# Optimization experiments

Hardware: AMD Instinct MI355X
Metric: run time of the kernel (lower is better)

Reference implementation:

```python
import jax, jax.numpy as jnp
import numpy as np
import math

B, S, HID = 2, 2048, 1024
NH, HD = 16, 64
MAX_SEQ = 65536  # RoPE base from RotaryEmbedding


def _rope_tables(seq_len, dim):
    inv_freq = 1.0 / (MAX_SEQ ** (jnp.arange(0, dim, 2, dtype=jnp.float32) / dim))
    t = jnp.arange(seq_len, dtype=jnp.float32)
    freqs = jnp.einsum('i,j->ij', t, inv_freq)          # [S, dim/2]
    emb = jnp.concatenate([freqs, freqs], axis=-1)      # [S, dim]
    return jnp.cos(emb), jnp.sin(emb)


def _rotate_half(x):
    x1, x2 = jnp.split(x, 2, axis=-1)
    return jnp.concatenate([-x2, x1], axis=-1)


def setup_inputs() -> dict:
    key = jax.random.key(0)
    ks = jax.random.split(key, 9)
    std_qkv = 1.0 / math.sqrt(NH * HD)
    std_o = 1.0 / math.sqrt(HID)
    return {
        'input_embeds': jax.random.normal(ks[0], (B, S, HID), dtype=jnp.float32),
        'Wq': jax.random.normal(ks[1], (NH * HD, HID), dtype=jnp.float32) * std_qkv,
        'bq': jnp.zeros((NH * HD,), dtype=jnp.float32),
        'Wk': jax.random.normal(ks[2], (NH * HD, HID), dtype=jnp.float32) * std_qkv,
        'bk': jnp.zeros((NH * HD,), dtype=jnp.float32),
        'Wv': jax.random.normal(ks[3], (NH * HD, HID), dtype=jnp.float32) * std_qkv,
        'bv': jnp.zeros((NH * HD,), dtype=jnp.float32),
        'Wo': jax.random.normal(ks[4], (HID, NH * HD), dtype=jnp.float32) * std_o,
        'bo': jnp.zeros((HID,), dtype=jnp.float32),
    }


def reference(input_embeds, Wq, bq, Wk, bk, Wv, bv, Wo, bo):
    x = input_embeds
    b, s, _ = x.shape
    # QKV projections (torch Linear: x @ W.T + b)
    q = x @ Wq.T + bq
    k = x @ Wk.T + bk
    v = x @ Wv.T + bv
    # [B, S, NH*HD] -> [B, NH, S, HD]
    q = q.reshape(b, s, NH, HD).transpose(0, 2, 1, 3)
    k = k.reshape(b, s, NH, HD).transpose(0, 2, 1, 3)
    v = v.reshape(b, s, NH, HD).transpose(0, 2, 1, 3)
    # RoPE
    cos, sin = _rope_tables(s, HD)  # [S, HD]
    q = q * cos + _rotate_half(q) * sin
    k = k * cos + _rotate_half(k) * sin
    # SDPA (non-causal, no mask)
    scale = 1.0 / math.sqrt(HD)
    scores = jnp.einsum('bhqd,bhkd->bhqk', q, k) * scale
    attn = jax.nn.softmax(scores, axis=-1)
    out = jnp.einsum('bhqk,bhkd->bhqd', attn, v)
    # [B, NH, S, HD] -> [B, S, NH*HD]
    out = out.transpose(0, 2, 1, 3).reshape(b, s, NH * HD)
    return out @ Wo.T + bo
```

## Files before the change

### kernel.cpp

```cpp
#include <hip/hip_runtime.h>
#include <cstdint>
#include <cstddef>

#define S_LEN 2048
#define NHEAD 16
#define HDIM  64
#define HID_  1024

typedef short s8v  __attribute__((ext_vector_type(8)));
typedef short s4v  __attribute__((ext_vector_type(4)));
typedef float f4v  __attribute__((ext_vector_type(4)));
typedef float f16v __attribute__((ext_vector_type(16)));

__device__ __forceinline__ short f2b(float x) {
    union { float f; unsigned u; } a; a.f = x;
    unsigned r = a.u + 0x7fffu + ((a.u >> 16) & 1u);
    return (short)(r >> 16);
}
__device__ __forceinline__ float b2f(short x) {
    union { unsigned u; float f; } a; a.u = ((unsigned)(unsigned short)x) << 16;
    return a.f;
}

__device__ __forceinline__ void gload_lds16(const void* g, void* l) {
    __builtin_amdgcn_global_load_lds(
        (__attribute__((address_space(1))) void*)const_cast<void*>(g),
        (__attribute__((address_space(3))) void*)l, 16, 0, 0);
}

__device__ __forceinline__ unsigned cvtpk(float a, float b) {
    unsigned r;
    asm("v_cvt_pk_bf16_f32 %0, %1, %2" : "=v"(r) : "v"(a), "v"(b));
    return r;
}
__device__ __forceinline__ void plswap(unsigned& a, unsigned& b) {
    asm("v_permlane32_swap_b32 %0, %1" : "+v"(a), "+v"(b));
}

__global__ __launch_bounds__(256) void prep_kernel(
    const float* __restrict__ X,
    const float* __restrict__ Wq, const float* __restrict__ Wk,
    const float* __restrict__ Wv, const float* __restrict__ Wo,
    short* __restrict__ Xb, short* __restrict__ Wcat, short* __restrict__ Wob,
    float2* __restrict__ rtab)
{
    const int bid = blockIdx.x;
    if (bid < 8192) {
        const float* src;
        short* dst;
        int i;
        if (bid < 4096) {
            src = X; dst = Xb; i = bid * 256 + threadIdx.x;
        } else {
            int w = (bid - 4096) >> 10;
            src = (w == 0) ? Wq : (w == 1) ? Wk : (w == 2) ? Wv : Wo;
            dst = (w < 3) ? (Wcat + (size_t)w * 1048576) : Wob;
            i = ((bid - 4096) & 1023) * 256 + threadIdx.x;
        }
        float4 v = reinterpret_cast<const float4*>(src)[i];
        s4v o;
        o[0] = f2b(v.x); o[1] = f2b(v.y); o[2] = f2b(v.z); o[3] = f2b(v.w);
        reinterpret_cast<s4v*>(dst)[i] = o;
    } else {
        int idx = (bid - 8192) * 256 + threadIdx.x;
        int s = idx >> 5, j = idx & 31;
        float inv = exp2f(-0.5f * (float)j);
        float ang = (float)s * inv;
        float2 cs; cs.x = cosf(ang); cs.y = sinf(ang);
        rtab[idx] = cs;
    }
}

__global__ __launch_bounds__(256) void gemm_qkv(
    const short* __restrict__ A, const short* __restrict__ Bw,
    const float* __restrict__ bq, const float* __restrict__ bk,
    const float* __restrict__ bv,
    short* __restrict__ Qo, short* __restrict__ Ko, short* __restrict__ Vo,
    const float2* __restrict__ rtab)
{
    __shared__ short Asl[2][128 * 32];
    __shared__ short Bsl[2][128 * 32];
    const int t = threadIdx.x;
    const int lane = t & 63;
    const int l15 = lane & 15, l4 = lane >> 4;
    const int wid = t >> 6;
    const int blk = blockIdx.x;
    const int x = blk & 7, j = blk >> 3;
    const int tn = (x * 3 + j % 3) * 128;
    const int tm = (j / 3) * 128;
    const int K = 1024;
    const int wrow = (wid >> 1) * 64, wcol = (wid & 1) * 64;

    f4v acc[4][4];
#pragma unroll
    for (int i = 0; i < 4; ++i)
#pragma unroll
        for (int jj = 0; jj < 4; ++jj) acc[i][jj] = (f4v){0.f, 0.f, 0.f, 0.f};

    const int r0 = t >> 2;
    const int c0 = (t & 3) * 8;
    const int wbase = (t & ~63) * 8;

#define QSTAGE(buf, kt) do { const int k0_ = (kt) << 5;                            \
        gload_lds16(A  + (size_t)(tm + r0)      * K + k0_ + c0, &Asl[buf][wbase]);        \
        gload_lds16(A  + (size_t)(tm + 64 + r0) * K + k0_ + c0, &Asl[buf][2048 + wbase]); \
        gload_lds16(Bw + (size_t)(tn + r0)      * K + k0_ + c0, &Bsl[buf][wbase]);        \
        gload_lds16(Bw + (size_t)(tn + 64 + r0) * K + k0_ + c0, &Bsl[buf][2048 + wbase]); \
    } while (0)

    QSTAGE(0, 0);
    int cur = 0;
    for (int kt = 0; kt < 32; ++kt) {
        if (kt < 31) {
            QSTAGE(cur ^ 1, kt + 1);
            asm volatile("s_waitcnt vmcnt(4)" ::: "memory");
        } else {
            asm volatile("s_waitcnt vmcnt(0)" ::: "memory");
        }
        __builtin_amdgcn_s_barrier();
        __builtin_amdgcn_sched_barrier(0);
        s8v af[4], bf[4];
#pragma unroll
        for (int i = 0; i < 4; ++i) {
            af[i] = *(const s8v*)&Asl[cur][(wrow + i * 16 + l15) * 32 + 8 * l4];
            bf[i] = *(const s8v*)&Bsl[cur][(wcol + i * 16 + l15) * 32 + 8 * l4];
        }
#pragma unroll
        for (int i = 0; i < 4; ++i)
#pragma unroll
            for (int jj = 0; jj < 4; ++jj)
                acc[i][jj] = __builtin_amdgcn_mfma_f32_16x16x32_bf16(af[i], bf[jj], acc[i][jj], 0, 0, 0);
        __builtin_amdgcn_s_barrier();
        cur ^= 1;
    }
#undef QSTAGE

    const int mode = tn >> 10;
    const float* bias = (mode == 0) ? bq : (mode == 1) ? bk : bv;
    short* outb = (mode == 0) ? Qo : (mode == 1) ? Ko : Vo;

    if (mode == 2) {
#pragma unroll
        for (int i = 0; i < 4; ++i) {
            int rowb = tm + wrow + i * 16 + l4 * 4;
            int b_ = rowb >> 11, s0 = rowb & 2047;
#pragma unroll
            for (int jj = 0; jj < 4; ++jj) {
                int col = tn + wcol + jj * 16 + l15;
                int cm = col & 1023;
                float bvv = bias[cm];
                int h = cm >> 6, d = col & 63;
                s4v o4;
#pragma unroll
                for (int r = 0; r < 4; ++r) o4[r] = f2b(acc[i][jj][r] + bvv);
                *(s4v*)&outb[((size_t)((b_ * NHEAD + h) * 64 + d)) * S_LEN + s0] = o4;
            }
        }
    } else {
        int h = ((tn & 1023) + wcol) >> 6;
        const float osc = (mode == 0) ? 0.180336880111f : 1.0f;
#pragma unroll
        for (int i = 0; i < 4; ++i) {
#pragma unroll
            for (int r = 0; r < 4; ++r) {
                int row = tm + wrow + i * 16 + l4 * 4 + r;
                int b_ = row >> 11, s = row & 2047;
                float2 cs0 = rtab[(s << 5) + l15];
                float2 cs1 = rtab[(s << 5) + 16 + l15];
#pragma unroll
                for (int jj = 0; jj < 4; ++jj) {
                    int col = tn + wcol + jj * 16 + l15;
                    int cm = col & 1023;
                    int d = col & 63;
                    float v  = acc[i][jj][r]     + bias[cm];
                    float vp = acc[i][jj ^ 2][r] + bias[cm ^ 32];
                    float2 cs = (jj & 1) ? cs1 : cs0;
                    float res = (d < 32) ? (v * cs.x - vp * cs.y)
                                         : (v * cs.x + vp * cs.y);
                    outb[(((size_t)(b_ * NHEAD + h) * S_LEN + s) << 6) + d] = f2b(res * osc);
                }
            }
        }
    }
}

__global__ __launch_bounds__(256) void gemm_o(
    const short* __restrict__ A, const short* __restrict__ Bw,
    const float* __restrict__ bias, float* __restrict__ outf)
{
    __shared__ short Asl[2][64 * 32];
    __shared__ short Bsl[2][128 * 32];
    const int t = threadIdx.x;
    const int lane = t & 63;
    const int l15 = lane & 15, l4 = lane >> 4;
    const int wid = t >> 6;
    const int blk = blockIdx.x;
    const int tn = (blk & 7) * 128;
    const int tm = (blk >> 3) * 64;
    const int K = 1024, N = 1024;
    const int wrow = (wid >> 1) * 32, wcol = (wid & 1) * 64;

    f4v acc[2][4];
#pragma unroll
    for (int i = 0; i < 2; ++i)
#pragma unroll
        for (int jj = 0; jj < 4; ++jj) acc[i][jj] = (f4v){0.f, 0.f, 0.f, 0.f};

    const int r0 = t >> 2;
    const int c0 = (t & 3) * 8;
    const int wbase = (t & ~63) * 8;

#define OSTAGE(buf, kt) do { const int k0_ = (kt) << 5;                            \
        gload_lds16(A  + (size_t)(tm + r0)      * K + k0_ + c0, &Asl[buf][wbase]);        \
        gload_lds16(Bw + (size_t)(tn + r0)      * K + k0_ + c0, &Bsl[buf][wbase]);        \
        gload_lds16(Bw + (size_t)(tn + 64 + r0) * K + k0_ + c0, &Bsl[buf][2048 + wbase]); \
    } while (0)

    OSTAGE(0, 0);
    int cur = 0;
    for (int kt = 0; kt < 32; ++kt) {
        if (kt < 31) {
            OSTAGE(cur ^ 1, kt + 1);
            asm volatile("s_waitcnt vmcnt(3)" ::: "memory");
        } else {
            asm volatile("s_waitcnt vmcnt(0)" ::: "memory");
        }
        __builtin_amdgcn_s_barrier();
        __builtin_amdgcn_sched_barrier(0);
        s8v af[2], bf[4];
#pragma unroll
        for (int i = 0; i < 2; ++i)
            af[i] = *(const s8v*)&Asl[cur][(wrow + i * 16 + l15) * 32 + 8 * l4];
#pragma unroll
        for (int jj = 0; jj < 4; ++jj)
            bf[jj] = *(const s8v*)&Bsl[cur][(wcol + jj * 16 + l15) * 32 + 8 * l4];
#pragma unroll
        for (int i = 0; i < 2; ++i)
#pragma unroll
            for (int jj = 0; jj < 4; ++jj)
                acc[i][jj] = __builtin_amdgcn_mfma_f32_16x16x32_bf16(af[i], bf[jj], acc[i][jj], 0, 0, 0);
        __builtin_amdgcn_s_barrier();
        cur ^= 1;
    }
#undef OSTAGE

#pragma unroll
    for (int i = 0; i < 2; ++i) {
        int rowb = tm + wrow + i * 16 + l4 * 4;
#pragma unroll
        for (int jj = 0; jj < 4; ++jj) {
            int col = tn + wcol + jj * 16 + l15;
            float bv = bias[col];
#pragma unroll
            for (int r = 0; r < 4; ++r)
                outf[(size_t)(rowb + r) * N + col] = acc[i][jj][r] + bv;
        }
    }
}

#define SWB(row, bofs) ((bofs) ^ (((row) & 7) << 4))

__global__ __launch_bounds__(256, 4) void attn_split(
    const short* __restrict__ Q, const short* __restrict__ K,
    const short* __restrict__ Vt,
    short* __restrict__ P0, short* __restrict__ P1, float2* __restrict__ ML)
{
    __shared__ short Kl[4096];
    __shared__ short Vl[4096];

    const int t = threadIdx.x, lane = t & 63;
    const int wid = t >> 6;
    const int q5 = lane & 31, hi = lane >> 5;

    const int blk = blockIdx.x;
    const int x = blk & 7, j = blk >> 3;
    const int bh = x * 4 + (j & 3);
    const int rest = j >> 2;
    const int qb = rest & 15, split = rest >> 4;
    const int kt0 = split * 16;

    const short* Qb = Q + (size_t)bh * S_LEN * 64;
    const char*  Kb = (const char*)(K  + (size_t)bh * S_LEN * 64);
    const char*  Vb = (const char*)(Vt + (size_t)bh * S_LEN * 64);
    const int qrow = qb * 128 + wid * 32 + q5;

    s8v qf[4];
#pragma unroll
    for (int sl = 0; sl < 4; ++sl)
        qf[sl] = *(const s8v*)&Qb[(size_t)qrow * 64 + sl * 16 + hi * 8];

    f16v oacc[2];
#pragma unroll
    for (int dt = 0; dt < 2; ++dt)
#pragma unroll
        for (int e = 0; e < 16; ++e) oacc[dt][e] = 0.f;
    float m2 = -1e30f, lsum = 0.f;

    const int skey  = t >> 3;
    const int sboff = (t & 7) * 16;
    const int sw    = SWB(skey, sboff);
    const size_t kgoff = (size_t)skey * 128  + sboff;
    const size_t vgoff = (size_t)skey * 4096 + sboff;
    char* KlB = (char*)Kl;
    char* VlB = (char*)Vl;
    const int w0 = skey * 128 + sw;
    const int w1 = w0 + 32 * 128;

    {
        const size_t kbB = (size_t)kt0 * 64 * 128;
        const size_t vbB = (size_t)kt0 * 64 * 2;
        s8v g0 = *(const s8v*)(Kb + kbB + kgoff);
        s8v g1 = *(const s8v*)(Kb + kbB + kgoff + 32 * 128);
        s8v g2 = *(const s8v*)(Vb + vbB + vgoff);
        s8v g3 = *(const s8v*)(Vb + vbB + vgoff + 32 * 4096);
        *(s8v*)(KlB + w0) = g0; *(s8v*)(KlB + w1) = g1;
        *(s8v*)(VlB + w0) = g2; *(s8v*)(VlB + w1) = g3;
    }
    __syncthreads();

    for (int kt = kt0; kt < kt0 + 16; ++kt) {
        s8v g0, g1, g2, g3;
        const bool pre = (kt < kt0 + 15);
        if (pre) {
            const size_t kbB = (size_t)(kt + 1) * 64 * 128;
            const size_t vbB = (size_t)(kt + 1) * 64 * 2;
            g0 = *(const s8v*)(Kb + kbB + kgoff);
            g1 = *(const s8v*)(Kb + kbB + kgoff + 32 * 128);
            g2 = *(const s8v*)(Vb + vbB + vgoff);
            g3 = *(const s8v*)(Vb + vbB + vgoff + 32 * 4096);
        }

        f16v sc[2];
#pragma unroll
        for (int e = 0; e < 16; ++e) { sc[0][e] = 0.f; sc[1][e] = 0.f; }
        {
            const int kr0 = q5, kr1 = 32 + q5;
            const char* kb0 = KlB + kr0 * 128;
            const char* kb1 = KlB + kr1 * 128;
            __builtin_amdgcn_s_setprio(1);
#pragma unroll
            for (int sl = 0; sl < 4; ++sl) {
                s8v kf0 = *(const s8v*)(kb0 + SWB(kr0, sl * 32 + hi * 16));
                s8v kf1 = *(const s8v*)(kb1 + SWB(kr1, sl * 32 + hi * 16));
                sc[0] = __builtin_amdgcn_mfma_f32_32x32x16_bf16(kf0, qf[sl], sc[0], 0, 0, 0);
                sc[1] = __builtin_amdgcn_mfma_f32_32x32x16_bf16(kf1, qf[sl], sc[1], 0, 0, 0);
            }
            __builtin_amdgcn_s_setprio(0);
        }

        float m8[8];
#pragma unroll
        for (int e = 0; e < 8; ++e)
            m8[e] = fmaxf(fmaxf(sc[0][e], sc[0][e + 8]), fmaxf(sc[1][e], sc[1][e + 8]));
        float pm = fmaxf(fmaxf(fmaxf(m8[0], m8[4]), fmaxf(m8[1], m8[5])),
                         fmaxf(fmaxf(m8[2], m8[6]), fmaxf(m8[3], m8[7])));
        pm = fmaxf(pm, __shfl_xor(pm, 32, 64));
        if (__any(pm > m2 + 8.0f)) {
            float m2n = fmaxf(m2, pm);
            float fr = __builtin_amdgcn_exp2f(m2 - m2n);
            lsum *= fr;
#pragma unroll
            for (int dt = 0; dt < 2; ++dt)
#pragma unroll
                for (int e = 0; e < 16; ++e) oacc[dt][e] *= fr;
            m2 = m2n;
        }
#pragma unroll
        for (int c = 0; c < 2; ++c)
#pragma unroll
            for (int e = 0; e < 16; ++e)
                sc[c][e] = __builtin_amdgcn_exp2f(sc[c][e] - m2);
        float sum8[8];
#pragma unroll
        for (int e = 0; e < 8; ++e)
            sum8[e] = (sc[0][e] + sc[0][e + 8]) + (sc[1][e] + sc[1][e + 8]);
        lsum += ((sum8[0] + sum8[4]) + (sum8[1] + sum8[5])) +
                ((sum8[2] + sum8[6]) + (sum8[3] + sum8[7]));

#pragma unroll
        for (int c = 0; c < 2; ++c) {
#pragma unroll
            for (int ks = 0; ks < 2; ++ks) {
                const int b0 = ks * 8;
                unsigned x0 = cvtpk(sc[c][b0 + 0], sc[c][b0 + 1]);
                unsigned y0 = cvtpk(sc[c][b0 + 4], sc[c][b0 + 5]);
                unsigned x1 = cvtpk(sc[c][b0 + 2], sc[c][b0 + 3]);
                unsigned y1 = cvtpk(sc[c][b0 + 6], sc[c][b0 + 7]);
                plswap(x0, y0);
                plswap(x1, y1);
                union { unsigned u[4]; s8v s; } pf;
                pf.u[0] = x0; pf.u[1] = x1; pf.u[2] = y0; pf.u[3] = y1;
                __builtin_amdgcn_s_setprio(1);
#pragma unroll
                for (int dt = 0; dt < 2; ++dt) {
                    const int vrow = dt * 32 + q5;
                    s8v vf = *(const s8v*)(VlB + vrow * 128 +
                                           SWB(vrow, c * 64 + ks * 32 + hi * 16));
                    oacc[dt] = __builtin_amdgcn_mfma_f32_32x32x16_bf16(vf, pf.s, oacc[dt], 0, 0, 0);
                }
                __builtin_amdgcn_s_setprio(0);
            }
        }

        __syncthreads();
        if (pre) {
            *(s8v*)(KlB + w0) = g0; *(s8v*)(KlB + w1) = g1;
            *(s8v*)(VlB + w0) = g2; *(s8v*)(VlB + w1) = g3;
        }
        __syncthreads();
    }

    float ls = lsum + __shfl_xor(lsum, 32, 64);
    float inv = 1.0f / ls;
    short* Pp = (split ? P1 : P0) + ((size_t)bh * S_LEN + qrow) * 64;
#pragma unroll
    for (int dt = 0; dt < 2; ++dt)
#pragma unroll
        for (int g = 0; g < 4; ++g) {
            s4v o4;
#pragma unroll
            for (int jj = 0; jj < 4; ++jj) o4[jj] = f2b(oacc[dt][g * 4 + jj] * inv);
            const int d0 = dt * 32 + g * 8 + hi * 4;
            *(s4v*)&Pp[d0] = o4;
        }
    if (hi == 0) {
        float2 ml; ml.x = m2; ml.y = ls;
        ML[(size_t)split * (32 * S_LEN) + bh * S_LEN + qrow] = ml;
    }
}

__global__ __launch_bounds__(256) void attn_combine(
    const short* __restrict__ P0, const short* __restrict__ P1,
    const float2* __restrict__ ML, short* __restrict__ Obf)
{
    int idx = blockIdx.x * 256 + threadIdx.x;
    int row = idx >> 3;
    int d0 = (idx & 7) * 8;
    float2 a = ML[row];
    float2 b = ML[32 * S_LEN + row];
    float m = fmaxf(a.x, b.x);
    float w0 = a.y * exp2f(a.x - m);
    float w1 = b.y * exp2f(b.x - m);
    float inv = 1.0f / (w0 + w1);
    w0 *= inv; w1 *= inv;
    s8v v0 = *(const s8v*)&P0[(size_t)row * 64 + d0];
    s8v v1 = *(const s8v*)&P1[(size_t)row * 64 + d0];
    s8v o;
#pragma unroll
    for (int e = 0; e < 8; ++e) o[e] = f2b(w0 * b2f(v0[e]) + w1 * b2f(v1[e]));
    int bh = row >> 11, s = row & 2047;
    int b_ = bh >> 4, h = bh & 15;
    *(s8v*)&Obf[((size_t)(b_ * S_LEN + s)) * HID_ + h * 64 + d0] = o;
}

extern "C" void kernel_launch(void* const* d_in, const int* in_sizes, int n_in,
                              void* d_out, int out_size, void* d_ws, size_t ws_size,
                              hipStream_t stream)
{
    const float* X  = (const float*)d_in[0];
    const float* Wq = (const float*)d_in[1];
    const float* bq = (const float*)d_in[2];
    const float* Wk = (const float*)d_in[3];
    const float* bk = (const float*)d_in[4];
    const float* Wv = (const float*)d_in[5];
    const float* bv = (const float*)d_in[6];
    const float* Wo = (const float*)d_in[7];
    const float* bo = (const float*)d_in[8];
    float* out = (float*)d_out;

    char* ws = (char*)d_ws;
    short*  Xb   = (short*) (ws);
    short*  Wcat = (short*) (ws + ( 8u << 20));
    short*  Wob  = (short*) (ws + (14u << 20));
    float2* rtab = (float2*)(ws + (16u << 20));
    short*  Qbh  = (short*) (ws + (17u << 20));
    short*  Kbh  = (short*) (ws + (25u << 20));
    short*  Vbh  = (short*) (ws + (33u << 20));
    short*  Obf  = (short*) (ws + (41u << 20));
    short*  P0   = (short*) (ws);
    short*  P1   = (short*) d_out;
    float2* ML   = (float2*)((char*)d_out + (8u << 20));

    prep_kernel<<<8448, 256, 0, stream>>>(X, Wq, Wk, Wv, Wo, Xb, Wcat, Wob, rtab);
    gemm_qkv<<<768, 256, 0, stream>>>(Xb, Wcat, bq, bk, bv, Qbh, Kbh, Vbh, rtab);
    attn_split<<<1024, 256, 0, stream>>>(Qbh, Kbh, Vbh, P0, P1, ML);
    attn_combine<<<2048, 256, 0, stream>>>(P0, P1, ML, Obf);
    gemm_o<<<512, 256, 0, stream>>>(Obf, Wob, bo, out);
}
```

Baseline: 151.3 us.

## Use 512-thread attention blocks and register-staged loads in QKV GEMM

The attention split kernel now runs 512 threads per block over 256 query rows, so each K/V tile in LDS is shared by eight waves and each thread stages one K and one V vector instead of two. Separately, the QKV GEMM drops its double-buffered global_load_lds pipeline in favour of prefetching into registers and writing a single LDS buffer between two barriers. The attention change aims to halve K/V load traffic per query row. The GEMM change adds an extra barrier per step and removes async LDS loads, which may hurt. Whether the attention kernel's internal indexing (skey, kgoff, vgoff, which are not shown) was updated to cover the full 64-row tile with 512 threads is unclear.

```diff
diff --git a/kernel.cpp b/kernel.cpp
--- a/kernel.cpp
+++ b/kernel.cpp
@@ -20,12 +20,6 @@
 __device__ __forceinline__ float b2f(short x) {
     union { unsigned u; float f; } a; a.u = ((unsigned)(unsigned short)x) << 16;
     return a.f;
-}
-
-__device__ __forceinline__ void gload_lds16(const void* g, void* l) {
-    __builtin_amdgcn_global_load_lds(
-        (__attribute__((address_space(1))) void*)const_cast<void*>(g),
-        (__attribute__((address_space(3))) void*)l, 16, 0, 0);
 }
 
 __device__ __forceinline__ unsigned cvtpk(float a, float b) {
@@ -78,8 +72,8 @@
     short* __restrict__ Qo, short* __restrict__ Ko, short* __restrict__ Vo,
     const float2* __restrict__ rtab)
 {
-    __shared__ short Asl[2][128 * 32];
-    __shared__ short Bsl[2][128 * 32];
+    __shared__ short Asl[128 * 32];
+    __shared__ short Bsl[128 * 32];
     const int t = threadIdx.x;
     const int lane = t & 63;
     const int l15 = lane & 15, l4 = lane >> 4;
@@ -99,41 +93,57 @@
 
     const int r0 = t >> 2;
     const int c0 = (t & 3) * 8;
-    const int wbase = (t & ~63) * 8;
-
-#define QSTAGE(buf, kt) do { const int k0_ = (kt) << 5;                            \
-        gload_lds16(A  + (size_t)(tm + r0)      * K + k0_ + c0, &Asl[buf][wbase]);        \
-        gload_lds16(A  + (size_t)(tm + 64 + r0) * K + k0_ + c0, &Asl[buf][2048 + wbase]); \
-        gload_lds16(Bw + (size_t)(tn + r0)      * K + k0_ + c0, &Bsl[buf][wbase]);        \
-        gload_lds16(Bw + (size_t)(tn + 64 + r0) * K + k0_ + c0, &Bsl[buf][2048 + wbase]); \
-    } while (0)
-
-    QSTAGE(0, 0);
-    int cur = 0;
+    short* wA0 = Asl + t * 8;
+    short* wA1 = Asl + 2048 * 8 / 8 * 8;
+    (void)wA1;
+
+    const short* Ap0 = A  + (size_t)(tm + r0)      * K + c0;
+    const short* Ap1 = A  + (size_t)(tm + 64 + r0) * K + c0;
+    const short* Bp0 = Bw + (size_t)(tn + r0)      * K + c0;
+    const short* Bp1 = Bw + (size_t)(tn + 64 + r0) * K + c0;
+    short* wAlo = Asl + t * 8;
+    short* wAhi = Asl + 2048 + t * 8;
+    short* wBlo = Bsl + t * 8;
+    short* wBhi = Bsl + 2048 + t * 8;
+
+    {
+        s8v ga0 = *(const s8v*)(Ap0);
+        s8v ga1 = *(const s8v*)(Ap1);
+        s8v gb0 = *(const s8v*)(Bp0);
+        s8v gb1 = *(const s8v*)(Bp1);
+        *(s8v*)wAlo = ga0; *(s8v*)wAhi = ga1;
+        *(s8v*)wBlo = gb0; *(s8v*)wBhi = gb1;
+    }
+    __syncthreads();
+
     for (int kt = 0; kt < 32; ++kt) {
-        if (kt < 31) {
-            QSTAGE(cur ^ 1, kt + 1);
-            asm volatile("s_waitcnt vmcnt(4)" ::: "memory");
-        } else {
-            asm volatile("s_waitcnt vmcnt(0)" ::: "memory");
-        }
-        __builtin_amdgcn_s_barrier();
-        __builtin_amdgcn_sched_barrier(0);
+        s8v ga0, ga1, gb0, gb1;
+        const bool pre = (kt < 31);
+        if (pre) {
+            const int k0 = (kt + 1) << 5;
+            ga0 = *(const s8v*)(Ap0 + k0);
+            ga1 = *(const s8v*)(Ap1 + k0);
+            gb0 = *(const s8v*)(Bp0 + k0);
+            gb1 = *(const s8v*)(Bp1 + k0);
+        }
         s8v af[4], bf[4];
 #pragma unroll
         for (int i = 0; i < 4; ++i) {
-            af[i] = *(const s8v*)&Asl[cur][(wrow + i * 16 + l15) * 32 + 8 * l4];
-            bf[i] = *(const s8v*)&Bsl[cur][(wcol + i * 16 + l15) * 32 + 8 * l4];
+            af[i] = *(const s8v*)&Asl[(wrow + i * 16 + l15) * 32 + 8 * l4];
+            bf[i] = *(const s8v*)&Bsl[(wcol + i * 16 + l15) * 32 + 8 * l4];
         }
 #pragma unroll
         for (int i = 0; i < 4; ++i)
 #pragma unroll
             for (int jj = 0; jj < 4; ++jj)
                 acc[i][jj] = __builtin_amdgcn_mfma_f32_16x16x32_bf16(af[i], bf[jj], acc[i][jj], 0, 0, 0);
-        __builtin_amdgcn_s_barrier();
-        cur ^= 1;
-    }
-#undef QSTAGE
+        __syncthreads();
+        if (pre) {
+            *(s8v*)wAlo = ga0; *(s8v*)wAhi = ga1;
+            *(s8v*)wBlo = gb0; *(s8v*)wBhi = gb1;
+        }
+        __syncthreads();
+    }
 
     const int mode = tn >> 10;
     const float* bias = (mode == 0) ? bq : (mode == 1) ? bk : bv;
@@ -182,6 +192,12 @@
             }
         }
     }
+}
+
+__device__ __forceinline__ void gload_lds16(const void* g, void* l) {
+    __builtin_amdgcn_global_load_lds(
+        (__attribute__((address_space(1))) void*)const_cast<void*>(g),
+        (__attribute__((address_space(3))) void*)l, 16, 0, 0);
 }
 
 __global__ __launch_bounds__(256) void gemm_o(
@@ -260,7 +276,7 @@
 
 #define SWB(row, bofs) ((bofs) ^ (((row) & 7) << 4))
 
-__global__ __launch_bounds__(256, 4) void attn_split(
+__global__ __launch_bounds__(512) void attn_split(
     const short* __restrict__ Q, const short* __restrict__ K,
     const short* __restrict__ Vt,
     short* __restrict__ P0, short* __restrict__ P1, float2* __restrict__ ML)
@@ -276,13 +292,13 @@
     const int x = blk & 7, j = blk >> 3;
     const int bh = x * 4 + (j & 3);
     const int rest = j >> 2;
-    const int qb = rest & 15, split = rest >> 4;
+    const int qb = rest & 7, split = rest >> 3;
     const int kt0 = split * 16;
 
     const short* Qb = Q + (size_t)bh * S_LEN * 64;
     const char*  Kb = (const char*)(K  + (size_t)bh * S_LEN * 64);
     const char*  Vb = (const char*)(Vt + (size_t)bh * S_LEN * 64);
-    const int qrow = qb * 128 + wid * 32 + q5;
+    const int qrow = qb * 256 + wid * 32 + q5;
 
     s8v qf[4];
 #pragma unroll
@@ -304,30 +320,25 @@
     char* KlB = (char*)Kl;
     char* VlB = (char*)Vl;
     const int w0 = skey * 128 + sw;
-    const int w1 = w0 + 32 * 128;
 
     {
         const size_t kbB = (size_t)kt0 * 64 * 128;
         const size_t vbB = (size_t)kt0 * 64 * 2;
         s8v g0 = *(const s8v*)(Kb + kbB + kgoff);
-        s8v g1 = *(const s8v*)(Kb + kbB + kgoff + 32 * 128);
-        s8v g2 = *(const s8v*)(Vb + vbB + vgoff);
-        s8v g3 = *(const s8v*)(Vb + vbB + vgoff + 32 * 4096);
-        *(s8v*)(KlB + w0) = g0; *(s8v*)(KlB + w1) = g1;
-        *(s8v*)(VlB + w0) = g2; *(s8v*)(VlB + w1) = g3;
+        s8v g1 = *(const s8v*)(Vb + vbB + vgoff);
+        *(s8v*)(KlB + w0) = g0;
+        *(s8v*)(VlB + w0) = g1;
     }
     __syncthreads();
 
     for (int kt = kt0; kt < kt0 + 16; ++kt) {
-        s8v g0, g1, g2, g3;
+        s8v g0, g1;
         const bool pre = (kt < kt0 + 15);
         if (pre) {
             const size_t kbB = (size_t)(kt + 1) * 64 * 128;
             const size_t vbB = (size_t)(kt + 1) * 64 * 2;
             g0 = *(const s8v*)(Kb + kbB + kgoff);
-            g1 = *(const s8v*)(Kb + kbB + kgoff + 32 * 128);
-            g2 = *(const s8v*)(Vb + vbB + vgoff);
-            g3 = *(const s8v*)(Vb + vbB + vgoff + 32 * 4096);
+            g1 = *(const s8v*)(Vb + vbB + vgoff);
         }
 
         f16v sc[2];
@@ -404,8 +415,8 @@
 
         __syncthreads();
         if (pre) {
-            *(s8v*)(KlB + w0) = g0; *(s8v*)(KlB + w1) = g1;
-            *(s8v*)(VlB + w0) = g2; *(s8v*)(VlB + w1) = g3;
+            *(s8v*)(KlB + w0) = g0;
+            *(s8v*)(VlB + w0) = g1;
         }
         __syncthreads();
     }
@@ -483,7 +494,7 @@
 
     prep_kernel<<<8448, 256, 0, stream>>>(X, Wq, Wk, Wv, Wo, Xb, Wcat, Wob, rtab);
     gemm_qkv<<<768, 256, 0, stream>>>(Xb, Wcat, bq, bk, bv, Qbh, Kbh, Vbh, rtab);
-    attn_split<<<1024, 256, 0, stream>>>(Qbh, Kbh, Vbh, P0, P1, ML);
+    attn_split<<<512, 512, 0, stream>>>(Qbh, Kbh, Vbh, P0, P1, ML);
     attn_combine<<<2048, 256, 0, stream>>>(P0, P1, ML, Obf);
     gemm_o<<<512, 256, 0, stream>>>(Obf, Wob, bo, out);
 }
```

Result: faster. 146.4 us (-3.2%).
